# Kernel optimization log

Hardware: AMD Instinct MI355X
Metric: run time of the kernel (lower is better)

The kernel has to match this reference:

```python
import jax, jax.numpy as jnp
import numpy as np

P = 16          # patch size
NP = 14         # patches per side (224/16)
D = 128         # model dim (== dim_head, 1 head)
DEPTH = 7
KNN_LAYER = 6   # memorizing_layers = (depth-1,)
M = 8192        # max_knn_memories
TOPK = 32       # num_retrieved_memories
SCALE = D ** -0.5
EPS = 1e-5


def _ln(x, g, b):
    mu = x.mean(-1, keepdims=True)
    var = ((x - mu) ** 2).mean(-1, keepdims=True)
    return (x - mu) / jnp.sqrt(var + EPS) * g + b


def setup_inputs() -> dict:
    key = jax.random.key(0)
    ks = jax.random.split(key, 10)
    rn = lambda k, shape, s=0.02: jax.random.normal(k, shape, jnp.float32) * s
    return {
        "x": jax.random.normal(ks[0], (32, 3, 224, 224), jnp.float32),
        "patch_w": rn(ks[1], (3 * P * P, D)),
        "patch_b": jnp.zeros((D,), jnp.float32),
        "ln1_g": jnp.ones((DEPTH, D), jnp.float32),
        "ln1_b": jnp.zeros((DEPTH, D), jnp.float32),
        "qkv_w": rn(ks[2], (DEPTH, D, 3 * D)),
        "qkv_b": jnp.zeros((DEPTH, 3 * D), jnp.float32),
        "out_w": rn(ks[3], (DEPTH, D, D)),
        "out_b": jnp.zeros((DEPTH, D), jnp.float32),
        "ln2_g": jnp.ones((DEPTH, D), jnp.float32),
        "ln2_b": jnp.zeros((DEPTH, D), jnp.float32),
        "ff1_w": rn(ks[4], (DEPTH, D, 4 * D)),
        "ff1_b": jnp.zeros((DEPTH, 4 * D), jnp.float32),
        "ff2_w": rn(ks[5], (DEPTH, 4 * D, D)),
        "ff2_b": jnp.zeros((DEPTH, D), jnp.float32),
        "lnf_g": jnp.ones((D,), jnp.float32),
        "lnf_b": jnp.zeros((D,), jnp.float32),
        "knn_k": jax.random.normal(ks[6], (32, M, D), jnp.float32),
        "knn_v": jax.random.normal(ks[7], (32, M, D), jnp.float32),
        "head_w": rn(ks[8], (D, 1000)),
        "head_b": jnp.zeros((1000,), jnp.float32),
    }


def reference(x, patch_w, patch_b, ln1_g, ln1_b, qkv_w, qkv_b, out_w, out_b,
              ln2_g, ln2_b, ff1_w, ff1_b, ff2_w, ff2_b, lnf_g, lnf_b,
              knn_k, knn_v, head_w, head_b):
    B = x.shape[0]
    # patchify: [B,3,224,224] -> [B,196,768]
    p = x.reshape(B, 3, NP, P, NP, P).transpose(0, 2, 4, 1, 3, 5).reshape(B, NP * NP, 3 * P * P)
    h = p @ patch_w + patch_b  # [B,196,128]
    for i in range(DEPTH):
        y = _ln(h, ln1_g[i], ln1_b[i])
        qkv = y @ qkv_w[i] + qkv_b[i]
        q, k, v = jnp.split(qkv, 3, axis=-1)
        sim = jnp.einsum('bnd,bmd->bnm', q, k) * SCALE  # local attention logits
        if i == KNN_LAYER:
            # kNN retrieval from external memory: top-k over 8192 memories per query
            msim = jnp.einsum('bnd,bmd->bnm', q, knn_k) * SCALE  # [B,196,8192]
            mvals, midx = jax.lax.top_k(msim, TOPK)               # [B,196,32]
            mv = jnp.take_along_axis(knn_v[:, None, :, :], midx[..., None], axis=2)  # [B,196,32,128]
            attn = jax.nn.softmax(jnp.concatenate([mvals, sim], axis=-1), axis=-1)
            am, al = attn[..., :TOPK], attn[..., TOPK:]
            o = jnp.einsum('bnk,bnkd->bnd', am, mv) + jnp.einsum('bnm,bmd->bnd', al, v)
        else:
            o = jnp.einsum('bnm,bmd->bnd', jax.nn.softmax(sim, axis=-1), v)
        h = h + o @ out_w[i] + out_b[i]
        y = _ln(h, ln2_g[i], ln2_b[i])
        h = h + jax.nn.gelu(y @ ff1_w[i] + ff1_b[i]) @ ff2_w[i] + ff2_b[i]
    feats = _ln(h, lnf_g, lnf_b).mean(axis=1)  # global mean pool -> [B,128]
    return feats @ head_w + head_b             # logits [B,1000]
```

## Files before the change

kernel.cpp:

```cpp
#include <hip/hip_runtime.h>
#include <hip/hip_fp16.h>

typedef unsigned short u16;
typedef __attribute__((ext_vector_type(8))) short short8;
typedef __attribute__((ext_vector_type(4))) float floatx4;

#define ATT_SCALE 0.08838834764831845f

__device__ __forceinline__ u16 f2bf(float f) {
  unsigned u = __float_as_uint(f);
  u += 0x7FFFu + ((u >> 16) & 1u);
  return (u16)(u >> 16);
}

__device__ __forceinline__ unsigned bfpack(float a, float b) {
  unsigned ua = __float_as_uint(a);
  ua += 0x7FFFu + ((ua >> 16) & 1u);
  unsigned ub = __float_as_uint(b);
  ub += 0x7FFFu + ((ub >> 16) & 1u);
  return __builtin_amdgcn_perm(ub, ua, 0x07060302u);
}

__device__ __forceinline__ float wsum(float v) {
#pragma unroll
  for (int m = 32; m >= 1; m >>= 1) v += __shfl_xor(v, m);
  return v;
}
__device__ __forceinline__ float wmaxr(float v) {
#pragma unroll
  for (int m = 32; m >= 1; m >>= 1) v = fmaxf(v, __shfl_xor(v, m));
  return v;
}

__device__ __forceinline__ float unpack_sc(unsigned p) {
  unsigned mono = p & 0xFFFFE000u;
  unsigned ub = (mono & 0x80000000u) ? (mono ^ 0x80000000u) : ~mono;
  return __uint_as_float(ub);
}

template <int EPI, bool BT>
__global__ __launch_bounds__(256) void gemm_k(
    const u16* __restrict__ A, int lda, long sA,
    const u16* __restrict__ B, int ldb, long sB, int Kb,
    const float* __restrict__ bias,
    const float* __restrict__ add, long sAdd,
    void* __restrict__ Cv, int ldc, long sC,
    int M, int N, int K, float alpha) {
  __shared__ u16 As[128][40];
  __shared__ u16 Bs[64][40];
  const int tid = threadIdx.x;
  const int m0 = blockIdx.x * 128, n0 = blockIdx.y * 64;
  const int bz = blockIdx.z;
  A += (long)bz * sA;
  B += (long)bz * sB;
  const int w = tid >> 6, lane = tid & 63;
  const int wr = w & 1, wc = w >> 1;
  const int lr = lane & 15, lk = (lane >> 4) * 8;
  floatx4 zf = {0.f, 0.f, 0.f, 0.f};
  floatx4 acc[4][2];
#pragma unroll
  for (int i = 0; i < 4; i++)
#pragma unroll
    for (int j = 0; j < 2; j++) acc[i][j] = zf;

  for (int k0 = 0; k0 < K; k0 += 32) {
#pragma unroll
    for (int t = 0; t < 2; t++) {
      int task = tid + t * 256;
      int r = task >> 2, k8 = (task & 3) * 8;
      short8 v = {0, 0, 0, 0, 0, 0, 0, 0};
      if (m0 + r < M) v = *(const short8*)(A + (long)(m0 + r) * lda + k0 + k8);
      *(short8*)&As[r][k8] = v;
    }
    if (!BT) {
      int r = tid >> 2, k8 = (tid & 3) * 8;
      short8 v = {0, 0, 0, 0, 0, 0, 0, 0};
      if (n0 + r < N) v = *(const short8*)(B + (long)(n0 + r) * ldb + k0 + k8);
      *(short8*)&Bs[r][k8] = v;
    } else {
#pragma unroll
      for (int t = 0; t < 8; t++) {
        int task = tid + t * 256;
        int n = task & 63, kk = task >> 6;
        u16 v = 0;
        if (k0 + kk < Kb && n0 + n < N) v = B[(long)(k0 + kk) * ldb + n0 + n];
        Bs[n][kk] = v;
      }
    }
    __syncthreads();
    short8 af[4], bfr[2];
#pragma unroll
    for (int i = 0; i < 4; i++) af[i] = *(const short8*)&As[wr * 64 + i * 16 + lr][lk];
#pragma unroll
    for (int j = 0; j < 2; j++) bfr[j] = *(const short8*)&Bs[wc * 32 + j * 16 + lr][lk];
#pragma unroll
    for (int i = 0; i < 4; i++)
#pragma unroll
      for (int j = 0; j < 2; j++)
        acc[i][j] = __builtin_amdgcn_mfma_f32_16x16x32_bf16(af[i], bfr[j], acc[i][j], 0, 0, 0);
    __syncthreads();
  }
#pragma unroll
  for (int i = 0; i < 4; i++) {
#pragma unroll
    for (int j = 0; j < 2; j++) {
      int gn = n0 + wc * 32 + j * 16 + lr;
#pragma unroll
      for (int r = 0; r < 4; r++) {
        int gm = m0 + wr * 64 + i * 16 + (lane >> 4) * 4 + r;
        if (gm < M && gn < N) {
          float v = acc[i][j][r];
          float bi = bias ? bias[gn] : 0.f;
          long co = (long)bz * sC + (long)gm * ldc + gn;
          if (EPI == 0) {
            ((float*)Cv)[co] = v * alpha + bi;
          } else if (EPI == 1) {
            ((u16*)Cv)[co] = f2bf(v + bi);
          } else if (EPI == 2) {
            float t = v + bi;
            float g = 0.5f * t * (1.f + tanhf(0.7978845608028654f * (t + 0.044715f * t * t * t)));
            ((u16*)Cv)[co] = f2bf(g);
          } else if (EPI == 3) {
            ((float*)Cv)[co] = add[(long)gm * ldc + gn] + v + bi;
          } else if (EPI == 4) {
            ((float*)Cv)[co] = v * alpha;
          } else {
            float t = v + (add ? add[(long)bz * sAdd + (long)gm * ldc + gn] : 0.f);
            ((u16*)Cv)[co] = f2bf(t);
          }
        }
      }
    }
  }
}

template <int EPI>
__global__ __launch_bounds__(256) void lngemm_k(
    const float* __restrict__ H, const float* __restrict__ g,
    const float* __restrict__ bb, const u16* __restrict__ B,
    const float* __restrict__ bias, u16* __restrict__ C, int ldc, int N) {
  __shared__ u16 As[128][136];
  __shared__ u16 Bs[64][136];
  __shared__ float stats[128][4];
  const int tid = threadIdx.x;
  const int m0 = blockIdx.x * 128, n0 = blockIdx.y * 64;
#pragma unroll
  for (int t = 0; t < 4; t++) {
    int task = tid + t * 256;
    int rb = task >> 4, c8 = (task & 15) * 8;
    short8 v = *(const short8*)(B + (long)(n0 + rb) * 128 + c8);
    *(short8*)&Bs[rb][c8] = v;
  }
  const int row = tid >> 1, half = tid & 1;
  float4 xv[16];
  const float* hp = H + (long)(m0 + row) * 128 + half * 64;
  float s1 = 0.f, s2 = 0.f;
#pragma unroll
  for (int t = 0; t < 16; t++) {
    xv[t] = *(const float4*)(hp + t * 4);
    s1 += xv[t].x + xv[t].y + xv[t].z + xv[t].w;
    s2 += xv[t].x * xv[t].x + xv[t].y * xv[t].y + xv[t].z * xv[t].z + xv[t].w * xv[t].w;
  }
  stats[row][half * 2] = s1;
  stats[row][half * 2 + 1] = s2;
  __syncthreads();
  float fs1 = stats[row][0] + stats[row][2];
  float fs2 = stats[row][1] + stats[row][3];
  float mu = fs1 * 0.0078125f;
  float var = fs2 * 0.0078125f - mu * mu;
  float rs = rsqrtf(var + 1e-5f);
  const float* gp = g + half * 64;
  const float* bp = bb + half * 64;
#pragma unroll
  for (int t = 0; t < 16; t++) {
    float4 gv = *(const float4*)(gp + t * 4);
    float4 bv = *(const float4*)(bp + t * 4);
    ushort4 o;
    o.x = f2bf((xv[t].x - mu) * rs * gv.x + bv.x);
    o.y = f2bf((xv[t].y - mu) * rs * gv.y + bv.y);
    o.z = f2bf((xv[t].z - mu) * rs * gv.z + bv.z);
    o.w = f2bf((xv[t].w - mu) * rs * gv.w + bv.w);
    *(ushort4*)&As[row][half * 64 + t * 4] = o;
  }
  __syncthreads();
  const int w = tid >> 6, lane = tid & 63;
  const int wr = w & 1, wc = w >> 1;
  const int lr = lane & 15, lk = (lane >> 4) * 8;
  floatx4 zf = {0.f, 0.f, 0.f, 0.f};
  floatx4 acc[4][2];
#pragma unroll
  for (int i = 0; i < 4; i++)
#pragma unroll
    for (int j = 0; j < 2; j++) acc[i][j] = zf;
#pragma unroll
  for (int kc = 0; kc < 4; kc++) {
    short8 afr[4], bfr[2];
#pragma unroll
    for (int i = 0; i < 4; i++) afr[i] = *(const short8*)&As[wr * 64 + i * 16 + lr][kc * 32 + lk];
#pragma unroll
    for (int j = 0; j < 2; j++) bfr[j] = *(const short8*)&Bs[wc * 32 + j * 16 + lr][kc * 32 + lk];
#pragma unroll
    for (int i = 0; i < 4; i++)
#pragma unroll
      for (int j = 0; j < 2; j++)
        acc[i][j] = __builtin_amdgcn_mfma_f32_16x16x32_bf16(afr[i], bfr[j], acc[i][j], 0, 0, 0);
  }
#pragma unroll
  for (int i = 0; i < 4; i++) {
#pragma unroll
    for (int j = 0; j < 2; j++) {
      int gn = n0 + wc * 32 + j * 16 + lr;
#pragma unroll
      for (int r = 0; r < 4; r++) {
        int gm = m0 + wr * 64 + i * 16 + (lane >> 4) * 4 + r;
        float v = acc[i][j][r] + bias[gn];
        if (EPI == 2) {
          v = 0.5f * v * (1.f + tanhf(0.7978845608028654f * (v + 0.044715f * v * v * v)));
        }
        C[(long)gm * ldc + gn] = f2bf(v);
      }
    }
  }
}

__global__ __launch_bounds__(256) void attn_k(const u16* __restrict__ qkv,
                                              u16* __restrict__ obf) {
  __shared__ u16 qs[32][136];
  __shared__ float sc[32][228];
  __shared__ u16 P[32][232];
  __shared__ u16 Vs[128][40];
  const int tid = threadIdx.x, w = tid >> 6, lane = tid & 63;
  const int b = blockIdx.y, n0 = blockIdx.x * 28;
  const u16* qb = qkv + (long)b * 196 * 384;
  {
    int r = tid >> 3, c0 = (tid & 7) * 16;
    short8 z = {0, 0, 0, 0, 0, 0, 0, 0};
    short8 v0 = z, v1 = z;
    if (r < 28) {
      const u16* src = qb + (long)(n0 + r) * 384 + c0;
      v0 = *(const short8*)src;
      v1 = *(const short8*)(src + 8);
    }
    *(short8*)&qs[r][c0] = v0;
    *(short8*)&qs[r][c0 + 8] = v1;
  }
  __syncthreads();
  const int lr = lane & 15, lq = lane >> 4, lk = lq * 8;
  short8 qf[2][4];
#pragma unroll
  for (int m = 0; m < 2; m++)
#pragma unroll
    for (int kc = 0; kc < 4; kc++)
      qf[m][kc] = *(const short8*)&qs[m * 16 + lr][kc * 32 + lk];

  const u16* kb = qb + 128;
#pragma unroll 1
  for (int c = w; c < 13; c += 4) {
    int key0 = c * 16;
    short8 kf[4];
    const u16* kp = kb + (long)(key0 + lr) * 384;
#pragma unroll
    for (int kc = 0; kc < 4; kc++) kf[kc] = *(const short8*)(kp + kc * 32 + lk);
#pragma unroll
    for (int m = 0; m < 2; m++) {
      floatx4 acc = {0.f, 0.f, 0.f, 0.f};
#pragma unroll
      for (int kc = 0; kc < 4; kc++)
        acc = __builtin_amdgcn_mfma_f32_16x16x32_bf16(qf[m][kc], kf[kc], acc, 0, 0, 0);
#pragma unroll
      for (int j = 0; j < 4; j++) sc[m * 16 + lq * 4 + j][key0 + lr] = acc[j];
    }
  }
  __syncthreads();
  {
    int r = tid >> 3, j0 = (tid & 7) * 28;
    if (r < 28) {
      float v[28];
      float mx = -1e30f;
#pragma unroll
      for (int i = 0; i < 28; i++) {
        int j = j0 + i;
        v[i] = (j < 196) ? sc[r][j] * ATT_SCALE : -1e30f;
        mx = fmaxf(mx, v[i]);
      }
#pragma unroll
      for (int m = 1; m <= 4; m <<= 1) mx = fmaxf(mx, __shfl_xor(mx, m));
      float s = 0.f;
#pragma unroll
      for (int i = 0; i < 28; i++) {
        v[i] = (j0 + i < 196) ? expf(v[i] - mx) : 0.f;
        s += v[i];
      }
#pragma unroll
      for (int m = 1; m <= 4; m <<= 1) s += __shfl_xor(s, m);
      float inv = 1.f / s;
#pragma unroll
      for (int i = 0; i < 28; i++) P[r][j0 + i] = f2bf(v[i] * inv);
    } else {
#pragma unroll
      for (int i = 0; i < 28; i++) P[r][j0 + i] = 0;
    }
  }
  __syncthreads();
  const int mtile = w & 1, nh = w >> 1;
  floatx4 acc[4];
#pragma unroll
  for (int t = 0; t < 4; t++) acc[t] = (floatx4){0.f, 0.f, 0.f, 0.f};
  const u16* vb = qb + 256;
#pragma unroll 1
  for (int kc = 0; kc < 7; kc++) {
    {
      int tok = tid >> 3, d0 = (tid & 7) * 16;
      int gt = kc * 32 + tok;
      short8 z = {0, 0, 0, 0, 0, 0, 0, 0};
      short8 v0 = z, v1 = z;
      if (gt < 196) {
        const u16* vp = vb + (long)gt * 384 + d0;
        v0 = *(const short8*)vp;
        v1 = *(const short8*)(vp + 8);
      }
      u16 tmp[16];
      *(short8*)tmp = v0;
      *(short8*)(tmp + 8) = v1;
#pragma unroll
      for (int i = 0; i < 16; i++) Vs[d0 + i][tok] = tmp[i];
    }
    __syncthreads();
    short8 pf = *(const short8*)&P[mtile * 16 + lr][kc * 32 + lk];
#pragma unroll
    for (int t = 0; t < 4; t++) {
      short8 vf = *(const short8*)&Vs[nh * 64 + t * 16 + lr][lk];
      acc[t] = __builtin_amdgcn_mfma_f32_16x16x32_bf16(pf, vf, acc[t], 0, 0, 0);
    }
    __syncthreads();
  }
#pragma unroll
  for (int t = 0; t < 4; t++) {
    int gn = nh * 64 + t * 16 + lr;
#pragma unroll
    for (int r = 0; r < 4; r++) {
      int rloc = mtile * 16 + lq * 4 + r;
      if (rloc < 28) obf[((long)b * 196 + n0 + rloc) * 128 + gn] = f2bf(acc[t][r]);
    }
  }
}

__global__ __launch_bounds__(256) void cvtw_k(
    const float* __restrict__ pw, const float* __restrict__ qw,
    const float* __restrict__ ow, const float* __restrict__ f1,
    const float* __restrict__ f2, u16* __restrict__ wbf) {
  int idx = blockIdx.x * 256 + threadIdx.x;
  float v;
  if (idx < 98304) {
    int n = idx / 768, k = idx % 768;
    v = pw[k * 128 + n];
  } else if (idx < 442368) {
    int rel = idx - 98304;
    int i = rel / 49152, r = rel % 49152, n = r / 128, k = r % 128;
    v = qw[((long)i * 128 + k) * 384 + n];
  } else if (idx < 557056) {
    int rel = idx - 442368;
    int i = rel / 16384, r = rel % 16384, n = r / 128, k = r % 128;
    v = ow[((long)i * 128 + k) * 128 + n];
  } else if (idx < 1015808) {
    int rel = idx - 557056;
    int i = rel / 65536, r = rel % 65536, n = r / 128, k = r % 128;
    v = f1[((long)i * 128 + k) * 512 + n];
  } else {
    int rel = idx - 1015808;
    int i = rel / 65536, r = rel % 65536, n = r / 512, k = r % 512;
    v = f2[((long)i * 512 + k) * 128 + n];
  }
  wbf[idx] = f2bf(v);
}

__global__ __launch_bounds__(256) void patchify_k(const float* __restrict__ x,
                                                  u16* __restrict__ p) {
  long idx = (long)blockIdx.x * 256 + threadIdx.x;
  int f = (int)(idx % 768);
  long bn = idx / 768;
  int n = (int)(bn % 196);
  int b = (int)(bn / 196);
  int c = f >> 8, ri = (f >> 4) & 15, cj = f & 15;
  int ph = n / 14, pw = n % 14;
  float v = x[(((long)b * 3 + c) * 224 + ph * 16 + ri) * 224 + pw * 16 + cj];
  p[idx] = f2bf(v);
}

__global__ __launch_bounds__(256) void knn_softmax_k(
    const float* __restrict__ sim, const float* __restrict__ mvals,
    u16* __restrict__ p, float* __restrict__ am) {
  int row = blockIdx.x * 4 + (threadIdx.x >> 6);
  int lane = threadIdx.x & 63;
  const float* sr = sim + (long)row * 224;
  float v[4];
#pragma unroll
  for (int t = 0; t < 4; t++) {
    int j = t * 64 + lane;
    v[t] = (j < 196) ? sr[j] : -1e30f;
  }
  float mvv = (lane < 32) ? mvals[(long)row * 32 + lane] : -1e30f;
  float mx = wmaxr(fmaxf(fmaxf(fmaxf(v[0], v[1]), fmaxf(v[2], v[3])), mvv));
  float e[4], s = 0.f;
#pragma unroll
  for (int t = 0; t < 4; t++) {
    int j = t * 64 + lane;
    e[t] = (j < 196) ? expf(v[t] - mx) : 0.f;
    s += e[t];
  }
  float em = (lane < 32) ? expf(mvv - mx) : 0.f;
  s = wsum(s + em);
  float inv = 1.f / s;
  u16* pr = p + (long)row * 224;
#pragma unroll
  for (int t = 0; t < 4; t++) {
    int j = t * 64 + lane;
    if (j < 224) pr[j] = f2bf(e[t] * inv);
  }
  if (lane < 32) am[(long)row * 32 + lane] = em * inv;
}

__global__ __launch_bounds__(256) void msim_topk_k(
    const u16* __restrict__ qkv, const float* __restrict__ knnk,
    unsigned* __restrict__ cand) {
  __shared__ u16 qs[64][136];
  const int tid = threadIdx.x, w = tid >> 6, lane = tid & 63;
  const int b = blockIdx.z, n0 = blockIdx.y * 49, kq0 = blockIdx.x * 1024;
  const u16* qb = qkv + (long)b * 196 * 384;
#pragma unroll
  for (int t = 0; t < 4; t++) {
    int task = tid + t * 256;
    int r = task >> 4, c8 = (task & 15) * 8;
    short8 v = {0, 0, 0, 0, 0, 0, 0, 0};
    if (r < 49) v = *(const short8*)(qb + (long)(n0 + r) * 384 + c8);
    *(short8*)&qs[r][c8] = v;
  }
  __syncthreads();
  const int lr = lane & 15, lq = lane >> 4, lk = lq * 8;
  short8 qf[4][4];
#pragma unroll
  for (int s = 0; s < 4; s++)
#pragma unroll
    for (int kc = 0; kc < 4; kc++)
      qf[s][kc] = *(const short8*)&qs[s * 16 + lr][kc * 32 + lk];

  unsigned st[4][8];
#pragma unroll
  for (int s = 0; s < 4; s++)
#pragma unroll
    for (int t = 0; t < 8; t++) st[s][t] = 0u;

  const float* kbase = knnk + ((long)b * 8192 + kq0 + lr) * 128 + lk;

  float4 raw[8];
  {
    const float* kp = kbase + (long)(w * 16) * 128;
#pragma unroll
    for (int kc = 0; kc < 4; kc++) {
      raw[kc * 2] = *(const float4*)(kp + kc * 32);
      raw[kc * 2 + 1] = *(const float4*)(kp + kc * 32 + 4);
    }
  }
#pragma unroll 1
  for (int c = 0; c < 16; c++) {
    float4 nraw[8];
    if (c < 15) {
      const float* kp = kbase + (long)(((c + 1) * 4 + w) * 16) * 128;
#pragma unroll
      for (int kc = 0; kc < 4; kc++) {
        nraw[kc * 2] = *(const float4*)(kp + kc * 32);
        nraw[kc * 2 + 1] = *(const float4*)(kp + kc * 32 + 4);
      }
    }
    short8 kf[4];
#pragma unroll
    for (int kc = 0; kc < 4; kc++) {
      int4 iv;
      iv.x = (int)bfpack(raw[kc * 2].x, raw[kc * 2].y);
      iv.y = (int)bfpack(raw[kc * 2].z, raw[kc * 2].w);
      iv.z = (int)bfpack(raw[kc * 2 + 1].x, raw[kc * 2 + 1].y);
      iv.w = (int)bfpack(raw[kc * 2 + 1].z, raw[kc * 2 + 1].w);
      kf[kc] = *(short8*)&iv;
    }
    const int kb = kq0 + (c * 4 + w) * 16 + lq * 4;
#pragma unroll
    for (int s = 0; s < 4; s++) {
      floatx4 acc = {0.f, 0.f, 0.f, 0.f};
#pragma unroll
      for (int kc = 0; kc < 4; kc++)
        acc = __builtin_amdgcn_mfma_f32_16x16x32_bf16(kf[kc], qf[s][kc], acc, 0, 0, 0);
#pragma unroll
      for (int r = 0; r < 4; r++) {
        float v = acc[r] * ATT_SCALE;
        unsigned u = __float_as_uint(v);
        unsigned mono = u ^ ((unsigned)((int)u >> 31) | 0x80000000u);
        unsigned x = (mono & 0xFFFFE000u) | (unsigned)(kb + r);
#pragma unroll
        for (int t = 0; t < 8; t++) {
          unsigned mx = max(st[s][t], x);
          x = min(st[s][t], x);
          st[s][t] = mx;
        }
      }
    }
    if (c < 15) {
#pragma unroll
      for (int i = 0; i < 8; i++) raw[i] = nraw[i];
    }
  }
#pragma unroll
  for (int s = 0; s < 4; s++) {
    int rloc = s * 16 + lr;
    if (rloc < 49) {
      unsigned* dst = cand + ((long)b * 196 + n0 + rloc) * 1024 + blockIdx.x * 128 + w * 32 + lq * 8;
#pragma unroll
      for (int t = 0; t < 8; t++) dst[t] = st[s][t];
    }
  }
}

__global__ __launch_bounds__(256) void topk_merge_k(
    const unsigned* __restrict__ cand, float* __restrict__ mvals,
    int* __restrict__ midx) {
  int row = blockIdx.x * 4 + (threadIdx.x >> 6);
  int lane = threadIdx.x & 63;
  const unsigned* cr = cand + (long)row * 1024;
  unsigned c[16];
#pragma unroll
  for (int t = 0; t < 16; t++) c[t] = cr[t * 64 + lane];
  float* mv = mvals + (long)row * 32;
  int* mi = midx + (long)row * 32;
  for (int r = 0; r < 32; r++) {
    unsigned lm = c[0];
#pragma unroll
    for (int t = 1; t < 16; t++) lm = max(lm, c[t]);
    unsigned gm = lm;
#pragma unroll
    for (int m = 32; m >= 1; m >>= 1) gm = max(gm, (unsigned)__shfl_xor((int)gm, m));
    bool has = false;
#pragma unroll
    for (int t = 0; t < 16; t++)
      if (!has && c[t] == gm) {
        c[t] = 0u;
        has = true;
      }
    if (has) {
      mv[r] = unpack_sc(gm);
      mi[r] = (int)(gm & 0x1FFFu);
    }
  }
}

__global__ __launch_bounds__(256) void knn_gather_k(
    const float* __restrict__ am, const int* __restrict__ ix,
    const float* __restrict__ kv, float* __restrict__ o32) {
  int row = blockIdx.x * 4 + (threadIdx.x >> 6);
  int lane = threadIdx.x & 63;
  int b = row / 196;
  const float* vb = kv + (long)b * 8192 * 128;
  const float* ar = am + (long)row * 32;
  const int* xr = ix + (long)row * 32;
  float a0 = 0.f, a1 = 0.f;
#pragma unroll 4
  for (int k = 0; k < 32; k++) {
    float wv = ar[k];
    int id = xr[k];
    float2 v = *(const float2*)&vb[(long)id * 128 + lane * 2];
    a0 += wv * v.x;
    a1 += wv * v.y;
  }
  float2 o;
  o.x = a0;
  o.y = a1;
  *(float2*)&o32[(long)row * 128 + lane * 2] = o;
}

__global__ __launch_bounds__(256) void final_k(
    const float* __restrict__ h, const float* __restrict__ g,
    const float* __restrict__ bb, const float* __restrict__ hw,
    const float* __restrict__ hb, float* __restrict__ out) {
  __shared__ float fw[4][128];
  __shared__ float feats[128];
  int tid = threadIdx.x, w = tid >> 6, lane = tid & 63;
  int b = blockIdx.x;
  float2 gv = *(const float2*)&g[lane * 2];
  float2 bv = *(const float2*)&bb[lane * 2];
  float a0 = 0.f, a1 = 0.f;
  for (int r = w; r < 196; r += 4) {
    float2 x = *(const float2*)&h[((long)b * 196 + r) * 128 + lane * 2];
    float mu = wsum(x.x + x.y) * 0.0078125f;
    float d0 = x.x - mu, d1 = x.y - mu;
    float var = wsum(d0 * d0 + d1 * d1) * 0.0078125f;
    float rs = 1.f / sqrtf(var + 1e-5f);
    a0 += d0 * rs * gv.x + bv.x;
    a1 += d1 * rs * gv.y + bv.y;
  }
  fw[w][lane * 2] = a0;
  fw[w][lane * 2 + 1] = a1;
  __syncthreads();
  if (tid < 128) feats[tid] = (fw[0][tid] + fw[1][tid] + fw[2][tid] + fw[3][tid]) * (1.f / 196.f);
  __syncthreads();
  for (int o = tid; o < 1000; o += 256) {
    float acc = hb[o];
    for (int d = 0; d < 128; d++) acc += feats[d] * hw[d * 1000 + o];
    out[(long)b * 1000 + o] = acc;
  }
}

extern "C" void kernel_launch(void* const* d_in, const int* in_sizes, int n_in,
                              void* d_out, int out_size, void* d_ws, size_t ws_size,
                              hipStream_t stream) {
  (void)in_sizes; (void)n_in; (void)out_size; (void)ws_size;
  const float* x       = (const float*)d_in[0];
  const float* patch_w = (const float*)d_in[1];
  const float* patch_b = (const float*)d_in[2];
  const float* ln1_g   = (const float*)d_in[3];
  const float* ln1_b   = (const float*)d_in[4];
  const float* qkv_w   = (const float*)d_in[5];
  const float* qkv_b   = (const float*)d_in[6];
  const float* out_w   = (const float*)d_in[7];
  const float* out_b   = (const float*)d_in[8];
  const float* ln2_g   = (const float*)d_in[9];
  const float* ln2_b   = (const float*)d_in[10];
  const float* ff1_w   = (const float*)d_in[11];
  const float* ff1_b   = (const float*)d_in[12];
  const float* ff2_w   = (const float*)d_in[13];
  const float* ff2_b   = (const float*)d_in[14];
  const float* lnf_g   = (const float*)d_in[15];
  const float* lnf_b   = (const float*)d_in[16];
  const float* knn_k   = (const float*)d_in[17];
  const float* knn_v   = (const float*)d_in[18];
  const float* head_w  = (const float*)d_in[19];
  const float* head_b  = (const float*)d_in[20];

  char* ws = (char*)d_ws;
  size_t off = 0;
  u16* wbf = (u16*)(ws + off);        off += 2949120;
  u16* p_bf = (u16*)(ws + off);       off += 9633792;
  float* h = (float*)(ws + off);      off += 3211264;
  u16* qkvb = (u16*)(ws + off);       off += 4816896;
  u16* g_bf = (u16*)(ws + off);       off += 6422528;
  u16* o_bf = (u16*)(ws + off);       off += 1605632;
  float* o32 = (float*)(ws + off);    off += 3211264;
  float* simf = (float*)(ws + off);   off += 5619712;
  u16* pbf = (u16*)(ws + off);        off += 2809856;
  unsigned* cand = (unsigned*)(ws + off); off += 25690112;
  float* mvals = (float*)(ws + off);  off += 802816;
  int* midx = (int*)(ws + off);       off += 802816;
  float* amf = (float*)(ws + off);    off += 802816;

  dim3 blk(256);
  cvtw_k<<<5760, blk, 0, stream>>>(patch_w, qkv_w, out_w, ff1_w, ff2_w, wbf);
  patchify_k<<<18816, blk, 0, stream>>>(x, p_bf);
  gemm_k<0, false><<<dim3(49, 2, 1), blk, 0, stream>>>(
      p_bf, 768, 0, wbf, 768, 0, 768, patch_b, nullptr, 0, h, 128, 0, 6272, 128, 768, 1.f);

  for (int i = 0; i < 7; i++) {
    lngemm_k<1><<<dim3(49, 6), blk, 0, stream>>>(
        h, ln1_g + i * 128, ln1_b + i * 128, wbf + 98304 + i * 49152,
        qkv_b + i * 384, qkvb, 384, 384);
    if (i == 6) {
      msim_topk_k<<<dim3(8, 4, 32), blk, 0, stream>>>(qkvb, knn_k, cand);
      topk_merge_k<<<1568, blk, 0, stream>>>(cand, mvals, midx);
      gemm_k<4, false><<<dim3(2, 4, 32), blk, 0, stream>>>(
          qkvb, 384, (long)196 * 384, qkvb + 128, 384, (long)196 * 384, 128,
          nullptr, nullptr, 0, simf, 224, (long)196 * 224, 196, 196, 128, ATT_SCALE);
      knn_softmax_k<<<1568, blk, 0, stream>>>(simf, mvals, pbf, amf);
      knn_gather_k<<<1568, blk, 0, stream>>>(amf, midx, knn_v, o32);
      gemm_k<5, true><<<dim3(2, 2, 32), blk, 0, stream>>>(
          pbf, 224, (long)196 * 224, qkvb + 256, 384, (long)196 * 384, 196,
          nullptr, o32, (long)196 * 128, o_bf, 128, (long)196 * 128, 196, 128, 224, 1.f);
    } else {
      attn_k<<<dim3(7, 32), blk, 0, stream>>>(qkvb, o_bf);
    }
    gemm_k<3, false><<<dim3(49, 2, 1), blk, 0, stream>>>(
        o_bf, 128, 0, wbf + 442368 + i * 16384, 128, 0, 128, out_b + i * 128,
        h, 0, h, 128, 0, 6272, 128, 128, 1.f);
    lngemm_k<2><<<dim3(49, 8), blk, 0, stream>>>(
        h, ln2_g + i * 128, ln2_b + i * 128, wbf + 557056 + i * 65536,
        ff1_b + i * 512, g_bf, 512, 512);
    gemm_k<3, false><<<dim3(49, 2, 1), blk, 0, stream>>>(
        g_bf, 512, 0, wbf + 1015808 + i * 65536, 512, 0, 512, ff2_b + i * 128,
        h, 0, h, 128, 0, 6272, 128, 512, 1.f);
  }
  final_k<<<32, blk, 0, stream>>>(h, lnf_g, lnf_b, head_w, head_b, (float*)d_out);
}
```

Before: 1.059 ms.

## Fuse out-proj+LN2+FF1 and FF2+LN1+QKV per layer; shrink top-k candidates

The per-layer chain of out-projection, residual, LN2 and FF1 GEMM moves into one kernel, and FF2, residual, the next layer's LN1 and the QKV GEMM into another. Both use 64-row tiles and compute full-row LayerNorm statistics in shared memory. This drops separate launches and fp32 h round-trips through global memory, at the cost of redundant first-stage GEMM work across the two N-blocks and less parallelism per launch. The kNN top-k stage also keeps 6 instead of 8 candidates per lane. It moves the attention scale from the hot loop to the merge step and shrinks the candidate buffer.

```diff
diff --git a/kernel.cpp b/kernel.cpp
--- a/kernel.cpp
+++ b/kernel.cpp
@@ -36,6 +36,10 @@
   unsigned mono = p & 0xFFFFE000u;
   unsigned ub = (mono & 0x80000000u) ? (mono ^ 0x80000000u) : ~mono;
   return __uint_as_float(ub);
+}
+
+__device__ __forceinline__ float gelu_f(float t) {
+  return 0.5f * t * (1.f + tanhf(0.7978845608028654f * (t + 0.044715f * t * t * t)));
 }
 
 template <int EPI, bool BT>
@@ -114,14 +118,6 @@
           long co = (long)bz * sC + (long)gm * ldc + gn;
           if (EPI == 0) {
             ((float*)Cv)[co] = v * alpha + bi;
-          } else if (EPI == 1) {
-            ((u16*)Cv)[co] = f2bf(v + bi);
-          } else if (EPI == 2) {
-            float t = v + bi;
-            float g = 0.5f * t * (1.f + tanhf(0.7978845608028654f * (t + 0.044715f * t * t * t)));
-            ((u16*)Cv)[co] = f2bf(g);
-          } else if (EPI == 3) {
-            ((float*)Cv)[co] = add[(long)gm * ldc + gn] + v + bi;
           } else if (EPI == 4) {
             ((float*)Cv)[co] = v * alpha;
           } else {
@@ -134,7 +130,6 @@
   }
 }
 
-template <int EPI>
 __global__ __launch_bounds__(256) void lngemm_k(
     const float* __restrict__ H, const float* __restrict__ g,
     const float* __restrict__ bb, const u16* __restrict__ B,
@@ -186,12 +181,11 @@
   const int w = tid >> 6, lane = tid & 63;
   const int wr = w & 1, wc = w >> 1;
   const int lr = lane & 15, lk = (lane >> 4) * 8;
-  floatx4 zf = {0.f, 0.f, 0.f, 0.f};
   floatx4 acc[4][2];
 #pragma unroll
   for (int i = 0; i < 4; i++)
 #pragma unroll
-    for (int j = 0; j < 2; j++) acc[i][j] = zf;
+    for (int j = 0; j < 2; j++) acc[i][j] = (floatx4){0.f, 0.f, 0.f, 0.f};
 #pragma unroll
   for (int kc = 0; kc < 4; kc++) {
     short8 afr[4], bfr[2];
@@ -214,10 +208,270 @@
       for (int r = 0; r < 4; r++) {
         int gm = m0 + wr * 64 + i * 16 + (lane >> 4) * 4 + r;
         float v = acc[i][j][r] + bias[gn];
-        if (EPI == 2) {
-          v = 0.5f * v * (1.f + tanhf(0.7978845608028654f * (v + 0.044715f * v * v * v)));
+        C[(long)gm * ldc + gn] = f2bf(v);
+      }
+    }
+  }
+}
+
+__global__ __launch_bounds__(256) void blockB_k(
+    const u16* __restrict__ obf, const u16* __restrict__ WoT,
+    const float* __restrict__ ob, const float* __restrict__ h,
+    const float* __restrict__ g2, const float* __restrict__ b2,
+    const u16* __restrict__ W1T, const float* __restrict__ b1,
+    float* __restrict__ h2, u16* __restrict__ gbf) {
+  __shared__ u16 As[64][136];
+  __shared__ u16 Bs[128][136];
+  __shared__ float stats[64][2];
+  const int tid = threadIdx.x, w = tid >> 6, lane = tid & 63;
+  const int m0 = blockIdx.x * 64, nb = blockIdx.y;
+  const int wr = w & 1, wc = w >> 1;
+  const int lr = lane & 15, lq = lane >> 4, lk = lq * 8;
+  if (tid < 128) stats[tid >> 1][tid & 1] = 0.f;
+#pragma unroll
+  for (int t = 0; t < 4; t++) {
+    int u = tid + t * 256;
+    int r = u >> 4, c8 = (u & 15) * 8;
+    *(short8*)&As[r][c8] = *(const short8*)(obf + (long)(m0 + r) * 128 + c8);
+  }
+#pragma unroll
+  for (int t = 0; t < 8; t++) {
+    int u = tid + t * 256;
+    int r = u >> 4, c8 = (u & 15) * 8;
+    *(short8*)&Bs[r][c8] = *(const short8*)(WoT + (long)r * 128 + c8);
+  }
+  __syncthreads();
+  floatx4 acc1[2][4];
+#pragma unroll
+  for (int i = 0; i < 2; i++)
+#pragma unroll
+    for (int j = 0; j < 4; j++) acc1[i][j] = (floatx4){0.f, 0.f, 0.f, 0.f};
+#pragma unroll
+  for (int kc = 0; kc < 4; kc++) {
+    short8 a0 = *(const short8*)&As[wr * 32 + lr][kc * 32 + lk];
+    short8 a1 = *(const short8*)&As[wr * 32 + 16 + lr][kc * 32 + lk];
+#pragma unroll
+    for (int j = 0; j < 4; j++) {
+      short8 bf = *(const short8*)&Bs[wc * 64 + j * 16 + lr][kc * 32 + lk];
+      acc1[0][j] = __builtin_amdgcn_mfma_f32_16x16x32_bf16(a0, bf, acc1[0][j], 0, 0, 0);
+      acc1[1][j] = __builtin_amdgcn_mfma_f32_16x16x32_bf16(a1, bf, acc1[1][j], 0, 0, 0);
+    }
+  }
+#pragma unroll
+  for (int i = 0; i < 2; i++) {
+#pragma unroll
+    for (int r = 0; r < 4; r++) {
+      int rloc = wr * 32 + i * 16 + lq * 4 + r;
+      int grow = m0 + rloc;
+      float p1 = 0.f, p2 = 0.f;
+#pragma unroll
+      for (int j = 0; j < 4; j++) {
+        int gn = wc * 64 + j * 16 + lr;
+        float v = acc1[i][j][r] + ob[gn] + h[(long)grow * 128 + gn];
+        acc1[i][j][r] = v;
+        p1 += v;
+        p2 += v * v;
+        if (nb == 0) h2[(long)grow * 128 + gn] = v;
+      }
+      atomicAdd(&stats[rloc][0], p1);
+      atomicAdd(&stats[rloc][1], p2);
+    }
+  }
+  __syncthreads();
+#pragma unroll
+  for (int i = 0; i < 2; i++) {
+#pragma unroll
+    for (int r = 0; r < 4; r++) {
+      int rloc = wr * 32 + i * 16 + lq * 4 + r;
+      float mu = stats[rloc][0] * 0.0078125f;
+      float var = stats[rloc][1] * 0.0078125f - mu * mu;
+      float rs = rsqrtf(var + 1e-5f);
+#pragma unroll
+      for (int j = 0; j < 4; j++) {
+        int gn = wc * 64 + j * 16 + lr;
+        float y = (acc1[i][j][r] - mu) * rs * g2[gn] + b2[gn];
+        As[rloc][gn] = f2bf(y);
+      }
+    }
+  }
+  __syncthreads();
+  short8 af2[2][4];
+#pragma unroll
+  for (int i = 0; i < 2; i++)
+#pragma unroll
+    for (int kc = 0; kc < 4; kc++)
+      af2[i][kc] = *(const short8*)&As[wr * 32 + i * 16 + lr][kc * 32 + lk];
+#pragma unroll 1
+  for (int t = 0; t < 4; t++) {
+    int n0t = nb * 256 + t * 64;
+    __syncthreads();
+#pragma unroll
+    for (int u4 = 0; u4 < 4; u4++) {
+      int u = tid + u4 * 256;
+      int r = u >> 4, c8 = (u & 15) * 8;
+      *(short8*)&Bs[r][c8] = *(const short8*)(W1T + (long)(n0t + r) * 128 + c8);
+    }
+    __syncthreads();
+    floatx4 acc2[2][2];
+#pragma unroll
+    for (int i = 0; i < 2; i++)
+#pragma unroll
+      for (int j = 0; j < 2; j++) acc2[i][j] = (floatx4){0.f, 0.f, 0.f, 0.f};
+#pragma unroll
+    for (int kc = 0; kc < 4; kc++) {
+#pragma unroll
+      for (int j = 0; j < 2; j++) {
+        short8 bf = *(const short8*)&Bs[wc * 32 + j * 16 + lr][kc * 32 + lk];
+        acc2[0][j] = __builtin_amdgcn_mfma_f32_16x16x32_bf16(af2[0][kc], bf, acc2[0][j], 0, 0, 0);
+        acc2[1][j] = __builtin_amdgcn_mfma_f32_16x16x32_bf16(af2[1][kc], bf, acc2[1][j], 0, 0, 0);
+      }
+    }
+#pragma unroll
+    for (int i = 0; i < 2; i++) {
+#pragma unroll
+      for (int j = 0; j < 2; j++) {
+        int gng = n0t + wc * 32 + j * 16 + lr;
+#pragma unroll
+        for (int r = 0; r < 4; r++) {
+          int grow = m0 + wr * 32 + i * 16 + lq * 4 + r;
+          float v = gelu_f(acc2[i][j][r] + b1[gng]);
+          gbf[(long)grow * 512 + gng] = f2bf(v);
         }
-        C[(long)gm * ldc + gn] = f2bf(v);
+      }
+    }
+  }
+}
+
+__global__ __launch_bounds__(256) void blockC_k(
+    const u16* __restrict__ gbf, const u16* __restrict__ W2T,
+    const float* __restrict__ b2f, const float* __restrict__ h2,
+    const float* __restrict__ g1, const float* __restrict__ b1,
+    const u16* __restrict__ WqT, const float* __restrict__ bq,
+    float* __restrict__ h3, u16* __restrict__ qkvo, int last) {
+  __shared__ u16 As[64][136];
+  __shared__ u16 Bs[128][136];
+  __shared__ float stats[64][2];
+  const int tid = threadIdx.x, w = tid >> 6, lane = tid & 63;
+  const int m0 = blockIdx.x * 64, nb = blockIdx.y;
+  const int wr = w & 1, wc = w >> 1;
+  const int lr = lane & 15, lq = lane >> 4, lk = lq * 8;
+  if (tid < 128) stats[tid >> 1][tid & 1] = 0.f;
+  floatx4 acc1[2][4];
+#pragma unroll
+  for (int i = 0; i < 2; i++)
+#pragma unroll
+    for (int j = 0; j < 4; j++) acc1[i][j] = (floatx4){0.f, 0.f, 0.f, 0.f};
+#pragma unroll 1
+  for (int kb = 0; kb < 4; kb++) {
+    __syncthreads();
+#pragma unroll
+    for (int t = 0; t < 4; t++) {
+      int u = tid + t * 256;
+      int r = u >> 4, c8 = (u & 15) * 8;
+      *(short8*)&As[r][c8] = *(const short8*)(gbf + (long)(m0 + r) * 512 + kb * 128 + c8);
+    }
+#pragma unroll
+    for (int t = 0; t < 8; t++) {
+      int u = tid + t * 256;
+      int r = u >> 4, c8 = (u & 15) * 8;
+      *(short8*)&Bs[r][c8] = *(const short8*)(W2T + (long)r * 512 + kb * 128 + c8);
+    }
+    __syncthreads();
+#pragma unroll
+    for (int kc = 0; kc < 4; kc++) {
+      short8 a0 = *(const short8*)&As[wr * 32 + lr][kc * 32 + lk];
+      short8 a1 = *(const short8*)&As[wr * 32 + 16 + lr][kc * 32 + lk];
+#pragma unroll
+      for (int j = 0; j < 4; j++) {
+        short8 bf = *(const short8*)&Bs[wc * 64 + j * 16 + lr][kc * 32 + lk];
+        acc1[0][j] = __builtin_amdgcn_mfma_f32_16x16x32_bf16(a0, bf, acc1[0][j], 0, 0, 0);
+        acc1[1][j] = __builtin_amdgcn_mfma_f32_16x16x32_bf16(a1, bf, acc1[1][j], 0, 0, 0);
+      }
+    }
+  }
+#pragma unroll
+  for (int i = 0; i < 2; i++) {
+#pragma unroll
+    for (int r = 0; r < 4; r++) {
+      int rloc = wr * 32 + i * 16 + lq * 4 + r;
+      int grow = m0 + rloc;
+      float p1 = 0.f, p2 = 0.f;
+#pragma unroll
+      for (int j = 0; j < 4; j++) {
+        int gn = wc * 64 + j * 16 + lr;
+        float v = acc1[i][j][r] + b2f[gn] + h2[(long)grow * 128 + gn];
+        acc1[i][j][r] = v;
+        p1 += v;
+        p2 += v * v;
+        if (nb == 0) h3[(long)grow * 128 + gn] = v;
+      }
+      if (!last) {
+        atomicAdd(&stats[rloc][0], p1);
+        atomicAdd(&stats[rloc][1], p2);
+      }
+    }
+  }
+  if (last) return;
+  __syncthreads();
+#pragma unroll
+  for (int i = 0; i < 2; i++) {
+#pragma unroll
+    for (int r = 0; r < 4; r++) {
+      int rloc = wr * 32 + i * 16 + lq * 4 + r;
+      float mu = stats[rloc][0] * 0.0078125f;
+      float var = stats[rloc][1] * 0.0078125f - mu * mu;
+      float rs = rsqrtf(var + 1e-5f);
+#pragma unroll
+      for (int j = 0; j < 4; j++) {
+        int gn = wc * 64 + j * 16 + lr;
+        float y = (acc1[i][j][r] - mu) * rs * g1[gn] + b1[gn];
+        As[rloc][gn] = f2bf(y);
+      }
+    }
+  }
+  __syncthreads();
+  short8 af2[2][4];
+#pragma unroll
+  for (int i = 0; i < 2; i++)
+#pragma unroll
+    for (int kc = 0; kc < 4; kc++)
+      af2[i][kc] = *(const short8*)&As[wr * 32 + i * 16 + lr][kc * 32 + lk];
+#pragma unroll 1
+  for (int t = 0; t < 3; t++) {
+    int n0t = nb * 192 + t * 64;
+    __syncthreads();
+#pragma unroll
+    for (int u4 = 0; u4 < 4; u4++) {
+      int u = tid + u4 * 256;
+      int r = u >> 4, c8 = (u & 15) * 8;
+      *(short8*)&Bs[r][c8] = *(const short8*)(WqT + (long)(n0t + r) * 128 + c8);
+    }
+    __syncthreads();
+    floatx4 acc2[2][2];
+#pragma unroll
+    for (int i = 0; i < 2; i++)
+#pragma unroll
+      for (int j = 0; j < 2; j++) acc2[i][j] = (floatx4){0.f, 0.f, 0.f, 0.f};
+#pragma unroll
+    for (int kc = 0; kc < 4; kc++) {
+#pragma unroll
+      for (int j = 0; j < 2; j++) {
+        short8 bf = *(const short8*)&Bs[wc * 32 + j * 16 + lr][kc * 32 + lk];
+        acc2[0][j] = __builtin_amdgcn_mfma_f32_16x16x32_bf16(af2[0][kc], bf, acc2[0][j], 0, 0, 0);
+        acc2[1][j] = __builtin_amdgcn_mfma_f32_16x16x32_bf16(af2[1][kc], bf, acc2[1][j], 0, 0, 0);
+      }
+    }
+#pragma unroll
+    for (int i = 0; i < 2; i++) {
+#pragma unroll
+      for (int j = 0; j < 2; j++) {
+        int gng = n0t + wc * 32 + j * 16 + lr;
+#pragma unroll
+        for (int r = 0; r < 4; r++) {
+          int grow = m0 + wr * 32 + i * 16 + lq * 4 + r;
+          float v = acc2[i][j][r] + bq[gng];
+          qkvo[(long)grow * 384 + gng] = f2bf(v);
+        }
       }
     }
   }
@@ -444,11 +698,11 @@
     for (int kc = 0; kc < 4; kc++)
       qf[s][kc] = *(const short8*)&qs[s * 16 + lr][kc * 32 + lk];
 
-  unsigned st[4][8];
+  unsigned st[4][6];
 #pragma unroll
   for (int s = 0; s < 4; s++)
 #pragma unroll
-    for (int t = 0; t < 8; t++) st[s][t] = 0u;
+    for (int t = 0; t < 6; t++) st[s][t] = 0u;
 
   const float* kbase = knnk + ((long)b * 8192 + kq0 + lr) * 128 + lk;
 
@@ -491,12 +745,11 @@
         acc = __builtin_amdgcn_mfma_f32_16x16x32_bf16(kf[kc], qf[s][kc], acc, 0, 0, 0);
 #pragma unroll
       for (int r = 0; r < 4; r++) {
-        float v = acc[r] * ATT_SCALE;
-        unsigned u = __float_as_uint(v);
+        unsigned u = __float_as_uint(acc[r]);
         unsigned mono = u ^ ((unsigned)((int)u >> 31) | 0x80000000u);
         unsigned x = (mono & 0xFFFFE000u) | (unsigned)(kb + r);
 #pragma unroll
-        for (int t = 0; t < 8; t++) {
+        for (int t = 0; t < 6; t++) {
           unsigned mx = max(st[s][t], x);
           x = min(st[s][t], x);
           st[s][t] = mx;
@@ -512,9 +765,9 @@
   for (int s = 0; s < 4; s++) {
     int rloc = s * 16 + lr;
     if (rloc < 49) {
-      unsigned* dst = cand + ((long)b * 196 + n0 + rloc) * 1024 + blockIdx.x * 128 + w * 32 + lq * 8;
-#pragma unroll
-      for (int t = 0; t < 8; t++) dst[t] = st[s][t];
+      unsigned* dst = cand + ((long)b * 196 + n0 + rloc) * 768 + blockIdx.x * 96 + w * 24 + lq * 6;
+#pragma unroll
+      for (int t = 0; t < 6; t++) dst[t] = st[s][t];
     }
   }
 }
@@ -524,28 +777,28 @@
     int* __restrict__ midx) {
   int row = blockIdx.x * 4 + (threadIdx.x >> 6);
   int lane = threadIdx.x & 63;
-  const unsigned* cr = cand + (long)row * 1024;
-  unsigned c[16];
-#pragma unroll
-  for (int t = 0; t < 16; t++) c[t] = cr[t * 64 + lane];
+  const unsigned* cr = cand + (long)row * 768;
+  unsigned c[12];
+#pragma unroll
+  for (int t = 0; t < 12; t++) c[t] = cr[t * 64 + lane];
   float* mv = mvals + (long)row * 32;
   int* mi = midx + (long)row * 32;
   for (int r = 0; r < 32; r++) {
     unsigned lm = c[0];
 #pragma unroll
-    for (int t = 1; t < 16; t++) lm = max(lm, c[t]);
+    for (int t = 1; t < 12; t++) lm = max(lm, c[t]);
     unsigned gm = lm;
 #pragma unroll
     for (int m = 32; m >= 1; m >>= 1) gm = max(gm, (unsigned)__shfl_xor((int)gm, m));
     bool has = false;
 #pragma unroll
-    for (int t = 0; t < 16; t++)
+    for (int t = 0; t < 12; t++)
       if (!has && c[t] == gm) {
         c[t] = 0u;
         has = true;
       }
     if (has) {
-      mv[r] = unpack_sc(gm);
+      mv[r] = unpack_sc(gm) * ATT_SCALE;
       mi[r] = (int)(gm & 0x1FFFu);
     }
   }
@@ -638,27 +891,29 @@
   u16* wbf = (u16*)(ws + off);        off += 2949120;
   u16* p_bf = (u16*)(ws + off);       off += 9633792;
   float* h = (float*)(ws + off);      off += 3211264;
+  float* h2 = (float*)(ws + off);     off += 3211264;
   u16* qkvb = (u16*)(ws + off);       off += 4816896;
   u16* g_bf = (u16*)(ws + off);       off += 6422528;
   u16* o_bf = (u16*)(ws + off);       off += 1605632;
   float* o32 = (float*)(ws + off);    off += 3211264;
   float* simf = (float*)(ws + off);   off += 5619712;
   u16* pbf = (u16*)(ws + off);        off += 2809856;
-  unsigned* cand = (unsigned*)(ws + off); off += 25690112;
+  unsigned* cand = (unsigned*)(ws + off); off += 19267584;
   float* mvals = (float*)(ws + off);  off += 802816;
   int* midx = (int*)(ws + off);       off += 802816;
   float* amf = (float*)(ws + off);    off += 802816;
+
+  const int qkvT = 98304, outT = 442368, ff1T = 557056, ff2T = 1015808;
 
   dim3 blk(256);
   cvtw_k<<<5760, blk, 0, stream>>>(patch_w, qkv_w, out_w, ff1_w, ff2_w, wbf);
   patchify_k<<<18816, blk, 0, stream>>>(x, p_bf);
   gemm_k<0, false><<<dim3(49, 2, 1), blk, 0, stream>>>(
       p_bf, 768, 0, wbf, 768, 0, 768, patch_b, nullptr, 0, h, 128, 0, 6272, 128, 768, 1.f);
+  lngemm_k<<<dim3(49, 6), blk, 0, stream>>>(
+      h, ln1_g, ln1_b, wbf + qkvT, qkv_b, qkvb, 384, 384);
 
   for (int i = 0; i < 7; i++) {
-    lngemm_k<1><<<dim3(49, 6), blk, 0, stream>>>(
-        h, ln1_g + i * 128, ln1_b + i * 128, wbf + 98304 + i * 49152,
-        qkv_b + i * 384, qkvb, 384, 384);
     if (i == 6) {
       msim_topk_k<<<dim3(8, 4, 32), blk, 0, stream>>>(qkvb, knn_k, cand);
       topk_merge_k<<<1568, blk, 0, stream>>>(cand, mvals, midx);
@@ -673,15 +928,20 @@
     } else {
       attn_k<<<dim3(7, 32), blk, 0, stream>>>(qkvb, o_bf);
     }
-    gemm_k<3, false><<<dim3(49, 2, 1), blk, 0, stream>>>(
-        o_bf, 128, 0, wbf + 442368 + i * 16384, 128, 0, 128, out_b + i * 128,
-        h, 0, h, 128, 0, 6272, 128, 128, 1.f);
-    lngemm_k<2><<<dim3(49, 8), blk, 0, stream>>>(
-        h, ln2_g + i * 128, ln2_b + i * 128, wbf + 557056 + i * 65536,
-        ff1_b + i * 512, g_bf, 512, 512);
-    gemm_k<3, false><<<dim3(49, 2, 1), blk, 0, stream>>>(
-        g_bf, 512, 0, wbf + 1015808 + i * 65536, 512, 0, 512, ff2_b + i * 128,
-        h, 0, h, 128, 0, 6272, 128, 512, 1.f);
+    blockB_k<<<dim3(98, 2), blk, 0, stream>>>(
+        o_bf, wbf + outT + i * 16384, out_b + i * 128, h,
+        ln2_g + i * 128, ln2_b + i * 128, wbf + ff1T + i * 65536, ff1_b + i * 512,
+        h2, g_bf);
+    if (i < 6) {
+      blockC_k<<<dim3(98, 2), blk, 0, stream>>>(
+          g_bf, wbf + ff2T + i * 65536, ff2_b + i * 128, h2,
+          ln1_g + (i + 1) * 128, ln1_b + (i + 1) * 128,
+          wbf + qkvT + (i + 1) * 49152, qkv_b + (i + 1) * 384, h, qkvb, 0);
+    } else {
+      blockC_k<<<dim3(98, 1), blk, 0, stream>>>(
+          g_bf, wbf + ff2T + i * 65536, ff2_b + i * 128, h2,
+          ln1_g, ln1_b, wbf + qkvT, qkv_b, h, qkvb, 1);
+    }
   }
   final_k<<<32, blk, 0, stream>>>(h, lnf_g, lnf_b, head_w, head_b, (float*)d_out);
 }
```

After: 917.6 us. 13.3% less time.
